# Kernel optimization log

Hardware: AMD Instinct MI355X
Metric: run time of the kernel (lower is better)

Reference implementation:

```python
import jax, jax.numpy as jnp
import numpy as np

B, OUT, IN = 65536, 2048, 64


def setup_inputs() -> dict:
    key = jax.random.key(0)
    k1, k2, k3 = jax.random.split(key, 3)
    inp = jax.random.normal(k1, (B, IN), dtype=jnp.float32)
    # kaiming-uniform-ish init for centers, small uniform for log_sigmas
    bound_c = float(np.sqrt(6.0 / ((1 + 5.0) * IN)))
    centers = jax.random.uniform(k2, (OUT, IN), dtype=jnp.float32, minval=-bound_c, maxval=bound_c)
    bound_s = 1.0 / float(np.sqrt(IN))
    log_sigmas = jax.random.uniform(k3, (OUT,), dtype=jnp.float32, minval=-bound_s, maxval=bound_s)
    return {"input": inp, "centers": centers, "log_sigmas": log_sigmas}


def _rbf_gaussian(x, centers, log_sigmas):
    # squared Euclidean distance via the GEMM trick (avoids materializing [B, OUT, IN]):
    x2 = jnp.sum(x * x, axis=-1, keepdims=True)          # [B, 1]
    c2 = jnp.sum(centers * centers, axis=-1)              # [OUT]
    xc = jnp.einsum('bi,oi->bo', x, centers)              # [B, OUT]
    sq = jnp.maximum(x2 - 2.0 * xc + c2[None, :], 0.0)    # clamp tiny negatives
    distances = jnp.sqrt(sq) / jnp.exp(log_sigmas)[None, :]
    return jnp.exp(-(distances * distances))              # gaussian basis


def reference(input, centers, log_sigmas):
    return _rbf_gaussian(input, centers, log_sigmas)
```

## Files before the change

### kernel.cpp

```cpp
#include <hip/hip_runtime.h>
#include <cstdint>
#include <cstddef>

#define B_ROWS 65536
#define OUT_N  2048
#define IN_K   64
#define LOG2E  1.4426950408889634f

typedef __attribute__((ext_vector_type(8))) short bf16x8;
typedef __attribute__((ext_vector_type(4))) float f32x4;
typedef __attribute__((ext_vector_type(4))) short s16x4;

__device__ __forceinline__ unsigned short f2bf_rtn(float v) {
  unsigned u = __float_as_uint(v);
  u += 0x7fffu + ((u >> 16) & 1u);
  return (unsigned short)(u >> 16);
}
__device__ __forceinline__ float bf2f(unsigned short s) {
  return __uint_as_float(((unsigned)s) << 16);
}

__global__ __launch_bounds__(64) void rbf_pre(
    const float* __restrict__ centers, const float* __restrict__ log_sigmas,
    unsigned short* __restrict__ ch, unsigned short* __restrict__ cl,
    float* __restrict__ c2, float* __restrict__ iv) {
  const int o = blockIdx.x;
  const int lane = threadIdx.x;
  float v = centers[o * IN_K + lane];
  unsigned short h = f2bf_rtn(v);
  float hf = bf2f(h);
  unsigned short l = f2bf_rtn(v - hf);
  ch[o * IN_K + lane] = h;
  cl[o * IN_K + lane] = l;
  float s = v * v;
  #pragma unroll
  for (int off = 32; off > 0; off >>= 1) s += __shfl_down(s, off, 64);
  if (lane == 0) {
    c2[o] = s;
    float ls = log_sigmas[o];
    iv[o] = __builtin_amdgcn_exp2f(-2.0f * ls * LOG2E) * LOG2E;
  }
}

__global__ __launch_bounds__(256) void rbf_main(
    const float* __restrict__ x,
    const unsigned short* __restrict__ ch, const unsigned short* __restrict__ cl,
    const float* __restrict__ c2, const float* __restrict__ iv,
    float* __restrict__ out) {
  __shared__ unsigned short xh[64 * 72];
  __shared__ unsigned short xl[64 * 72];
  __shared__ float x2s[64];

  const int t = threadIdx.x;
  const int b0 = blockIdx.x * 64;

  if (t < 64) x2s[t] = 0.0f;
  __syncthreads();

  const f32x4* xv = (const f32x4*)(x + (size_t)b0 * IN_K);
  #pragma unroll
  for (int i = 0; i < 4; ++i) {
    int f4 = i * 256 + t;
    f32x4 v = xv[f4];
    int row = f4 >> 4;
    int col = (f4 & 15) * 4;
    s16x4 h, l;
    #pragma unroll
    for (int j = 0; j < 4; ++j) {
      unsigned short hh = f2bf_rtn(v[j]);
      h[j] = (short)hh;
      l[j] = (short)f2bf_rtn(v[j] - bf2f(hh));
    }
    *(s16x4*)(xh + row * 72 + col) = h;
    *(s16x4*)(xl + row * 72 + col) = l;
    atomicAdd(&x2s[row], v[0] * v[0] + v[1] * v[1] + v[2] * v[2] + v[3] * v[3]);
  }
  __syncthreads();

  const int lane = t & 63;
  const int w    = t >> 6;
  const int n    = lane & 15;
  const int quad = lane >> 4;
  const int kq   = quad * 8;

  for (int oc = 0; oc < OUT_N; oc += 256) {
    const int obase = oc + w * 64;
    #pragma unroll
    for (int mt = 0; mt < 4; ++mt) {
      const int o0 = obase + mt * 16;
      const int arow = o0 + n;
      bf16x8 ah0 = *(const bf16x8*)(ch + arow * IN_K + kq);
      bf16x8 ah1 = *(const bf16x8*)(ch + arow * IN_K + kq + 32);
      bf16x8 al0 = *(const bf16x8*)(cl + arow * IN_K + kq);
      bf16x8 al1 = *(const bf16x8*)(cl + arow * IN_K + kq + 32);
      f32x4 c2v = *(const f32x4*)(c2 + o0 + quad * 4);
      f32x4 ivv = *(const f32x4*)(iv + o0 + quad * 4);
      #pragma unroll
      for (int nt = 0; nt < 4; ++nt) {
        const int brow = nt * 16 + n;
        const unsigned short* bp  = xh + brow * 72 + kq;
        const unsigned short* bpl = xl + brow * 72 + kq;
        bf16x8 bh0 = *(const bf16x8*)(bp);
        bf16x8 bh1 = *(const bf16x8*)(bp + 32);
        bf16x8 bl0 = *(const bf16x8*)(bpl);
        bf16x8 bl1 = *(const bf16x8*)(bpl + 32);
        f32x4 acc = {0.0f, 0.0f, 0.0f, 0.0f};
        acc = __builtin_amdgcn_mfma_f32_16x16x32_bf16(ah0, bh0, acc, 0, 0, 0);
        acc = __builtin_amdgcn_mfma_f32_16x16x32_bf16(ah1, bh1, acc, 0, 0, 0);
        acc = __builtin_amdgcn_mfma_f32_16x16x32_bf16(ah0, bl0, acc, 0, 0, 0);
        acc = __builtin_amdgcn_mfma_f32_16x16x32_bf16(ah1, bl1, acc, 0, 0, 0);
        acc = __builtin_amdgcn_mfma_f32_16x16x32_bf16(al0, bh0, acc, 0, 0, 0);
        acc = __builtin_amdgcn_mfma_f32_16x16x32_bf16(al1, bh1, acc, 0, 0, 0);
        const float x2v = x2s[brow];
        f32x4 r;
        #pragma unroll
        for (int j = 0; j < 4; ++j) {
          float sq = x2v - 2.0f * acc[j] + c2v[j];
          sq = fmaxf(sq, 0.0f);
          r[j] = __builtin_amdgcn_exp2f(-sq * ivv[j]);
        }
        *(f32x4*)(out + (size_t)(b0 + brow) * OUT_N + o0 + quad * 4) = r;
      }
    }
  }
}

extern "C" void kernel_launch(void* const* d_in, const int* in_sizes, int n_in,
                              void* d_out, int out_size, void* d_ws, size_t ws_size,
                              hipStream_t stream) {
  (void)in_sizes; (void)n_in; (void)out_size; (void)ws_size;
  const float* x       = (const float*)d_in[0];
  const float* centers = (const float*)d_in[1];
  const float* ls      = (const float*)d_in[2];
  float* out = (float*)d_out;

  char* ws = (char*)d_ws;
  unsigned short* ch = (unsigned short*)(ws);
  unsigned short* cl = (unsigned short*)(ws + 262144);
  float* c2 = (float*)(ws + 524288);
  float* iv = (float*)(ws + 532480);

  rbf_pre<<<OUT_N, 64, 0, stream>>>(centers, ls, ch, cl, c2, iv);
  rbf_main<<<B_ROWS / 64, 256, 0, stream>>>(x, ch, cl, c2, iv, out);
}
```

Measured before the change: 646.9 us.

## Retile RBF kernel to 2D grid with register-resident center fragments

The main kernel now covers 256 batch rows and one 256-wide slice of outputs per block over a 2D grid, instead of 64 rows across all 2048 outputs. Each wave loads its center hi/lo fragments, c2 and inverse-sigma values into registers once and reuses them across 16 batch-row tiles, so it no longer reloads centers from global memory for every output chunk. The cost is that x tiles are converted and reduced 8 times (once per output slice), LDS use grows to about 74 KB, and register pressure rises under launch bounds of 2 blocks per CU. The output is written at the same volume, so the change mainly helps if center reloads or instruction overhead were limiting a write-bound kernel.

Result: faster. 580.0 us (-10.3%).

```diff
diff --git a/kernel.cpp b/kernel.cpp
--- a/kernel.cpp
+++ b/kernel.cpp
@@ -6,6 +6,9 @@
 #define OUT_N  2048
 #define IN_K   64
 #define LOG2E  1.4426950408889634f
+
+#define ROWS_B 256
+#define OC_B   256
 
 typedef __attribute__((ext_vector_type(8))) short bf16x8;
 typedef __attribute__((ext_vector_type(4))) float f32x4;
@@ -42,24 +45,25 @@
   }
 }
 
-__global__ __launch_bounds__(256) void rbf_main(
+__global__ __launch_bounds__(256, 2) void rbf_main(
     const float* __restrict__ x,
     const unsigned short* __restrict__ ch, const unsigned short* __restrict__ cl,
     const float* __restrict__ c2, const float* __restrict__ iv,
     float* __restrict__ out) {
-  __shared__ unsigned short xh[64 * 72];
-  __shared__ unsigned short xl[64 * 72];
-  __shared__ float x2s[64];
+  __shared__ unsigned short xh[ROWS_B * 72];
+  __shared__ unsigned short xl[ROWS_B * 72];
+  __shared__ float x2s[ROWS_B];
 
   const int t = threadIdx.x;
-  const int b0 = blockIdx.x * 64;
+  const int b0  = blockIdx.x * ROWS_B;
+  const int ocb = blockIdx.y * OC_B;
 
-  if (t < 64) x2s[t] = 0.0f;
+  x2s[t] = 0.0f;
   __syncthreads();
 
   const f32x4* xv = (const f32x4*)(x + (size_t)b0 * IN_K);
   #pragma unroll
-  for (int i = 0; i < 4; ++i) {
+  for (int i = 0; i < 16; ++i) {
     int f4 = i * 256 + t;
     f32x4 v = xv[f4];
     int row = f4 >> 4;
@@ -83,44 +87,49 @@
   const int quad = lane >> 4;
   const int kq   = quad * 8;
 
-  for (int oc = 0; oc < OUT_N; oc += 256) {
-    const int obase = oc + w * 64;
+  const int obase = ocb + w * 64;
+
+  bf16x8 AH0[4], AH1[4], AL0[4], AL1[4];
+  f32x4  C2[4], IV[4];
+  #pragma unroll
+  for (int mt = 0; mt < 4; ++mt) {
+    const int arow = obase + mt * 16 + n;
+    AH0[mt] = *(const bf16x8*)(ch + arow * IN_K + kq);
+    AH1[mt] = *(const bf16x8*)(ch + arow * IN_K + kq + 32);
+    AL0[mt] = *(const bf16x8*)(cl + arow * IN_K + kq);
+    AL1[mt] = *(const bf16x8*)(cl + arow * IN_K + kq + 32);
+    C2[mt]  = *(const f32x4*)(c2 + obase + mt * 16 + quad * 4);
+    IV[mt]  = *(const f32x4*)(iv + obase + mt * 16 + quad * 4);
+  }
+
+  #pragma unroll 2
+  for (int nt = 0; nt < 16; ++nt) {
+    const int brow = nt * 16 + n;
+    const unsigned short* bp  = xh + brow * 72 + kq;
+    const unsigned short* bpl = xl + brow * 72 + kq;
+    bf16x8 bh0 = *(const bf16x8*)(bp);
+    bf16x8 bh1 = *(const bf16x8*)(bp + 32);
+    bf16x8 bl0 = *(const bf16x8*)(bpl);
+    bf16x8 bl1 = *(const bf16x8*)(bpl + 32);
+    const float x2v = x2s[brow];
+    float* prow = out + (size_t)(b0 + brow) * OUT_N + obase + quad * 4;
     #pragma unroll
     for (int mt = 0; mt < 4; ++mt) {
-      const int o0 = obase + mt * 16;
-      const int arow = o0 + n;
-      bf16x8 ah0 = *(const bf16x8*)(ch + arow * IN_K + kq);
-      bf16x8 ah1 = *(const bf16x8*)(ch + arow * IN_K + kq + 32);
-      bf16x8 al0 = *(const bf16x8*)(cl + arow * IN_K + kq);
-      bf16x8 al1 = *(const bf16x8*)(cl + arow * IN_K + kq + 32);
-      f32x4 c2v = *(const f32x4*)(c2 + o0 + quad * 4);
-      f32x4 ivv = *(const f32x4*)(iv + o0 + quad * 4);
+      f32x4 acc = {0.0f, 0.0f, 0.0f, 0.0f};
+      acc = __builtin_amdgcn_mfma_f32_16x16x32_bf16(AH0[mt], bh0, acc, 0, 0, 0);
+      acc = __builtin_amdgcn_mfma_f32_16x16x32_bf16(AH1[mt], bh1, acc, 0, 0, 0);
+      acc = __builtin_amdgcn_mfma_f32_16x16x32_bf16(AH0[mt], bl0, acc, 0, 0, 0);
+      acc = __builtin_amdgcn_mfma_f32_16x16x32_bf16(AH1[mt], bl1, acc, 0, 0, 0);
+      acc = __builtin_amdgcn_mfma_f32_16x16x32_bf16(AL0[mt], bh0, acc, 0, 0, 0);
+      acc = __builtin_amdgcn_mfma_f32_16x16x32_bf16(AL1[mt], bh1, acc, 0, 0, 0);
+      f32x4 r;
       #pragma unroll
-      for (int nt = 0; nt < 4; ++nt) {
-        const int brow = nt * 16 + n;
-        const unsigned short* bp  = xh + brow * 72 + kq;
-        const unsigned short* bpl = xl + brow * 72 + kq;
-        bf16x8 bh0 = *(const bf16x8*)(bp);
-        bf16x8 bh1 = *(const bf16x8*)(bp + 32);
-        bf16x8 bl0 = *(const bf16x8*)(bpl);
-        bf16x8 bl1 = *(const bf16x8*)(bpl + 32);
-        f32x4 acc = {0.0f, 0.0f, 0.0f, 0.0f};
-        acc = __builtin_amdgcn_mfma_f32_16x16x32_bf16(ah0, bh0, acc, 0, 0, 0);
-        acc = __builtin_amdgcn_mfma_f32_16x16x32_bf16(ah1, bh1, acc, 0, 0, 0);
-        acc = __builtin_amdgcn_mfma_f32_16x16x32_bf16(ah0, bl0, acc, 0, 0, 0);
-        acc = __builtin_amdgcn_mfma_f32_16x16x32_bf16(ah1, bl1, acc, 0, 0, 0);
-        acc = __builtin_amdgcn_mfma_f32_16x16x32_bf16(al0, bh0, acc, 0, 0, 0);
-        acc = __builtin_amdgcn_mfma_f32_16x16x32_bf16(al1, bh1, acc, 0, 0, 0);
-        const float x2v = x2s[brow];
-        f32x4 r;
-        #pragma unroll
-        for (int j = 0; j < 4; ++j) {
-          float sq = x2v - 2.0f * acc[j] + c2v[j];
-          sq = fmaxf(sq, 0.0f);
-          r[j] = __builtin_amdgcn_exp2f(-sq * ivv[j]);
-        }
-        *(f32x4*)(out + (size_t)(b0 + brow) * OUT_N + o0 + quad * 4) = r;
+      for (int j = 0; j < 4; ++j) {
+        float sq = x2v - 2.0f * acc[j] + C2[mt][j];
+        sq = fmaxf(sq, 0.0f);
+        r[j] = __builtin_amdgcn_exp2f(-sq * IV[mt][j]);
       }
+      *(f32x4*)(prow + mt * 16) = r;
     }
   }
 }
@@ -141,5 +150,5 @@
   float* iv = (float*)(ws + 532480);
 
   rbf_pre<<<OUT_N, 64, 0, stream>>>(centers, ls, ch, cl, c2, iv);
-  rbf_main<<<B_ROWS / 64, 256, 0, stream>>>(x, ch, cl, c2, iv, out);
+  rbf_main<<<dim3(B_ROWS / ROWS_B, OUT_N / OC_B), 256, 0, stream>>>(x, ch, cl, c2, iv, out);
 }
```
